# Kernel tuning notes

Hardware: AMD Instinct MI355X
Metric: run time of the kernel (lower is better)

The kernel has to match this reference:

```python
import jax, jax.numpy as jnp
import numpy as np

QN, QP = -8.0, 7.0  # int4: Qn=-2**3, Qp=2**3-1
LOG2E = 1.4426950408889634  # 1/ln(2)

def round_ste(x):
    return x + jax.lax.stop_gradient(jnp.round(x) - x)

def sg(x):
    return jax.lax.stop_gradient(x)

def mean_var_int(x_int, scale=1024):
    """Serial integer running-mean/var recurrence over the last dim.
    x_int: (B,H,N,D) int32. Returns mu (int values, float32) and varn float32, shape (B,H,N,1).
    Matches the torch loop: m_i = m_{i-1} + (x_i-m_{i-1})*int(1024/(i+1))//1024,
    v_i = v_{i-1} + (x_i-m_{i-1})*(x_i-m_i), with m_0=x_0, v_0=0 (same as the general
    recurrence with m_{-1}=v_{-1}=0 since int(1024/1)=1024)."""
    D = x_int.shape[3]
    coef = jnp.array([scale // (i + 1) for i in range(D)], dtype=jnp.int32)
    xt = jnp.moveaxis(x_int, 3, 0)  # (D,B,H,N)
    z = jnp.zeros(x_int.shape[:3], jnp.int32)
    def step(carry, inp):
        m, v = carry
        xi, c = inp
        d = xi - m
        new_m = m + (d * c) // scale  # floor division, matches torch //
        new_v = v + d * (xi - new_m)
        return (new_m, new_v), None
    (m, v), _ = jax.lax.scan(step, (z, z), (xt, coef))
    mu = m[..., None].astype(jnp.float32)
    varn = v[..., None].astype(jnp.float32) / D
    return mu, varn

def q_attention_forward(x0, qkv_w, qkv_b, qkv_alpha, qkv_act_alpha,
                        proj_w, proj_b, proj_alpha, proj_act_alpha,
                        norm_q_w, norm_q_b, norm_k_w, norm_k_b,
                        q_alpha, k_alpha, v_alpha, attn_alpha,
                        num_heads=12):
    B, N, C = x0.shape
    H = num_heads
    hd = C // H
    head_scale = hd ** -0.5

    # input activation quantization (ActQ_v2 then .int())
    a_in = qkv_act_alpha.mean()
    x0_2b = sg(jnp.round(jnp.clip(x0 / a_in, QN, QP)))  # int-valued (B,N,C)

    # int4 qkv weight quantization (per-output-channel alpha), integer GEMM
    w_qkv = sg(jnp.round(jnp.clip(qkv_w / qkv_alpha[:, None], QN, QP)))  # (3C,C)
    qkv = jnp.einsum('bnc,oc->bno', x0_2b, w_qkv)
    bias_i = sg(jnp.trunc(qkv_b / a_in / qkv_alpha))  # bias.int()
    qkv = qkv + bias_i

    qkv = jnp.transpose(qkv.reshape(B, N, 3, H, hd), (2, 0, 3, 1, 4))
    q0, k0, v0 = qkv[0], qkv[1], qkv[2]  # (B,H,N,hd)
    alpha_r = qkv_alpha.reshape(3, H, 1, hd)

    # q branch: scaled integer mean/var norm + scaled quantization
    xq = q0 * alpha_r[0]
    mu_q, var_q = mean_var_int(xq.astype(jnp.int32))
    q1 = (xq - mu_q) / (jnp.sqrt(var_q) + 1e-5)
    aq = q_alpha.mean()
    q2 = sg(jnp.round(jnp.clip((q1 + norm_q_b / norm_q_w) * norm_q_w / aq, QN, QP)))

    # k branch
    xk = k0 * alpha_r[1]
    mu_k, var_k = mean_var_int(xk.astype(jnp.int32))
    k1 = (xk - mu_k) / (jnp.sqrt(var_k) + 1e-5)
    ak = k_alpha.mean()
    k2 = sg(jnp.round(jnp.clip((k1 + norm_k_b / norm_k_w) * norm_k_w / ak, QN, QP)))

    # v branch
    av = v_alpha.mean()
    v2 = sg(jnp.round(jnp.clip(v0 * (a_in * alpha_r[2]) / av, QN, QP)))

    # integer q @ k^T
    qk = jnp.einsum('bhqd,bhkd->bhqk', q2, k2)  # (B,H,N,N)

    # power-of-two softmax approximation: 2^floor(e) * (1 + frac(e))
    s = head_scale * aq * ak
    e = LOG2E * s * qk
    f = jnp.floor(e)
    attn_exp = jnp.exp2(f) * (1.0 + (e - f))
    am = attn_alpha.mean()
    attn_norm = attn_exp / attn_exp.sum(-1, keepdims=True)
    attn2 = sg(jnp.round(jnp.clip(attn_norm / am, QN, QP)))

    x1p = jnp.einsum('bhqk,bhkd->bhqd', attn2, v2)
    x1p = jnp.transpose(x1p, (0, 2, 1, 3)).reshape(B, N, C)

    # proj-act quantization (round_pass STE, no .int() here in torch)
    ap = proj_act_alpha.mean()
    x1_2b = round_ste(jnp.clip(x1p * (am * av) / ap, QN, QP))

    w_p = sg(jnp.round(jnp.clip(proj_w / proj_alpha[:, None], QN, QP)))  # w_q.int()
    x2 = jnp.einsum('bnc,oc->bno', x1_2b, w_p) * proj_alpha * ap + proj_b
    return x2

def setup_inputs() -> dict:
    key = jax.random.key(0)
    ks = jax.random.split(key, 17)
    B, N, C, H = 4, 1024, 768, 12
    u = lambda k, shape, lo, hi: jax.random.uniform(k, shape, jnp.float32, lo, hi)
    return {
        "x0": jax.random.normal(ks[0], (B, N, C), jnp.float32),
        "qkv_w": jax.random.normal(ks[1], (3 * C, C), jnp.float32) * 0.02,
        "qkv_b": jax.random.normal(ks[2], (3 * C,), jnp.float32),
        "qkv_alpha": u(ks[3], (3 * C,), 0.008, 0.012),
        "qkv_act_alpha": u(ks[4], (C,), 0.25, 0.35),
        "proj_w": jax.random.normal(ks[5], (C, C), jnp.float32) * 0.02,
        "proj_b": jax.random.normal(ks[6], (C,), jnp.float32) * 0.02,
        "proj_alpha": u(ks[7], (C,), 0.008, 0.012),
        "proj_act_alpha": u(ks[8], (C,), 0.008, 0.012),
        "norm_q_w": u(ks[9], (C // H,), 0.8, 1.2),
        "norm_q_b": jax.random.normal(ks[10], (C // H,), jnp.float32) * 0.1,
        "norm_k_w": u(ks[11], (C // H,), 0.8, 1.2),
        "norm_k_b": jax.random.normal(ks[12], (C // H,), jnp.float32) * 0.1,
        "q_alpha": u(ks[13], (H,), 0.25, 0.35),
        "k_alpha": u(ks[14], (H,), 0.25, 0.35),
        "v_alpha": u(ks[15], (H,), 0.15, 0.25),
        "attn_alpha": u(ks[16], (H,), 0.0008, 0.0015),
    }

def reference(x0, qkv_w, qkv_b, qkv_alpha, qkv_act_alpha,
              proj_w, proj_b, proj_alpha, proj_act_alpha,
              norm_q_w, norm_q_b, norm_k_w, norm_k_b,
              q_alpha, k_alpha, v_alpha, attn_alpha):
    return q_attention_forward(x0, qkv_w, qkv_b, qkv_alpha, qkv_act_alpha,
                               proj_w, proj_b, proj_alpha, proj_act_alpha,
                               norm_q_w, norm_q_b, norm_k_w, norm_k_b,
                               q_alpha, k_alpha, v_alpha, attn_alpha)
```

## Files before the change

### kernel.cpp

```cpp
#include <hip/hip_runtime.h>

typedef unsigned short u16;
typedef unsigned int u32;
typedef __attribute__((ext_vector_type(8))) u16 u16x8;
typedef __attribute__((ext_vector_type(8))) __bf16 bf16x8;
typedef __attribute__((ext_vector_type(4))) float f32x4;

#define LOG2E_F 1.4426950408889634f

__device__ __forceinline__ u16 f2bf(float f) {
  return (u16)(__float_as_uint(f) >> 16);
}
__device__ __forceinline__ float clip87(float x) {
  return fminf(fmaxf(x, -8.0f), 7.0f);
}

typedef const __attribute__((address_space(1))) u32* gp32;
typedef __attribute__((address_space(3))) u32* lp32;
__device__ __forceinline__ void gl16(const void* g, void* l) {
  __builtin_amdgcn_global_load_lds((gp32)g, (lp32)l, 16, 0, 0);
}

__global__ void k_scalars(const float* __restrict__ qkv_act_alpha,
                          const float* __restrict__ proj_act_alpha,
                          const float* __restrict__ q_alpha,
                          const float* __restrict__ k_alpha,
                          const float* __restrict__ v_alpha,
                          const float* __restrict__ attn_alpha,
                          float* __restrict__ scal) {
  int tid = threadIdx.x;
  int wave = tid >> 6, lane = tid & 63;
  if (wave < 6) {
    const float* src = nullptr; int n = 0;
    switch (wave) {
      case 0: src = qkv_act_alpha;  n = 768; break;
      case 1: src = q_alpha;        n = 12;  break;
      case 2: src = k_alpha;        n = 12;  break;
      case 3: src = v_alpha;        n = 12;  break;
      case 4: src = attn_alpha;     n = 12;  break;
      case 5: src = proj_act_alpha; n = 768; break;
    }
    double s = 0.0;
    for (int i = lane; i < n; i += 64) s += (double)src[i];
    s += __shfl_xor(s, 1);
    s += __shfl_xor(s, 2);
    s += __shfl_xor(s, 4);
    s += __shfl_xor(s, 8);
    s += __shfl_xor(s, 16);
    s += __shfl_xor(s, 32);
    if (lane == 0) scal[wave] = (float)(s / (double)n);
  }
  __syncthreads();
  if (tid == 0) {
    float aq = scal[1], ak = scal[2];
    float s_ = (0.125f * aq) * ak;
    scal[6] = LOG2E_F * s_;
    scal[7] = scal[4] * scal[3];
  }
}

__global__ __launch_bounds__(256) void k_quant_weights(
    const float* __restrict__ qkv_w, const float* __restrict__ qkv_alpha,
    const float* __restrict__ qkv_b, const float* __restrict__ proj_w,
    const float* __restrict__ proj_alpha, const float* __restrict__ scal,
    u16* __restrict__ wq, u16* __restrict__ wp, float* __restrict__ biasi) {
  int idx = blockIdx.x * 256 + threadIdx.x;
  const int T1 = 2304 * 768, T2 = 768 * 768;
  if (idx < T1) {
    int o = idx / 768;
    wq[idx] = f2bf(rintf(clip87(qkv_w[idx] / qkv_alpha[o])));
  } else if (idx < T1 + T2) {
    int j = idx - T1;
    int o = j / 768;
    wp[j] = f2bf(rintf(clip87(proj_w[j] / proj_alpha[o])));
  } else if (idx < T1 + T2 + 2304) {
    int o = idx - T1 - T2;
    biasi[o] = truncf((qkv_b[o] / scal[0]) / qkv_alpha[o]);
  }
}

__global__ __launch_bounds__(256) void k_quant_x0(const float* __restrict__ x0,
                                                  const float* __restrict__ scal,
                                                  u16* __restrict__ x0q) {
  int base = (blockIdx.x * 256 + threadIdx.x) * 8;
  float a = scal[0];
  f32x4 v0 = *(const f32x4*)&x0[base];
  f32x4 v1 = *(const f32x4*)&x0[base + 4];
  u16x8 o;
  #pragma unroll
  for (int j = 0; j < 4; j++) o[j] = f2bf(rintf(clip87(v0[j] / a)));
  #pragma unroll
  for (int j = 0; j < 4; j++) o[4 + j] = f2bf(rintf(clip87(v1[j] / a)));
  *(u16x8*)&x0q[base] = o;
}

#define BUF_A64(c) (smem_u16 + (c) * 4096)
#define BUF_B64(c) (smem_u16 + 8192 + (c) * 4096)

__device__ __forceinline__ void stage64(const u16* gAl, const u16* gBl, int K,
                                        u16* bufA, u16* bufB, int w) {
  gl16(gAl, bufA + (w * 16) * 64);
  gl16(gAl + (size_t)8 * K, bufA + (w * 16 + 8) * 64);
  gl16(gBl, bufB + (w * 16) * 64);
  gl16(gBl + (size_t)8 * K, bufB + (w * 16 + 8) * 64);
}

__device__ __forceinline__ void gemm64(const u16* __restrict__ A,
                                       const u16* __restrict__ Bt, int K,
                                       int m0, int n0, u16* smem_u16,
                                       int lane, int wave, f32x4 acc[2][2]) {
  int rsub = lane >> 3;
  int jsrc = (lane & 7) ^ rsub;
  const u16* gAl = A + (size_t)(m0 + wave * 16 + rsub) * K + jsrc * 8;
  const u16* gBl = Bt + (size_t)(n0 + wave * 16 + rsub) * K + jsrc * 8;

  int arow = (wave >> 1) * 32 + (lane & 15);
  int brow = (wave & 1) * 32 + (lane & 15);
  int nsteps = K / 64;

  stage64(gAl, gBl, K, BUF_A64(0), BUF_B64(0), wave);
  __syncthreads();
  for (int t = 0; t < nsteps; t++) {
    int cur = t & 1;
    if (t + 1 < nsteps)
      stage64(gAl + (t + 1) * 64, gBl + (t + 1) * 64, K,
              BUF_A64(cur ^ 1), BUF_B64(cur ^ 1), wave);
    const u16* bA = BUF_A64(cur);
    const u16* bB = BUF_B64(cur);
    #pragma unroll
    for (int kk = 0; kk < 2; kk++) {
      int jj = ((kk * 4 + (lane >> 4)) ^ (lane & 7)) * 8;
      bf16x8 af0 = *(const bf16x8*)&bA[arow * 64 + jj];
      bf16x8 af1 = *(const bf16x8*)&bA[(arow + 16) * 64 + jj];
      bf16x8 bf0 = *(const bf16x8*)&bB[brow * 64 + jj];
      bf16x8 bf1 = *(const bf16x8*)&bB[(brow + 16) * 64 + jj];
      acc[0][0] = __builtin_amdgcn_mfma_f32_16x16x32_bf16(af0, bf0, acc[0][0], 0, 0, 0);
      acc[0][1] = __builtin_amdgcn_mfma_f32_16x16x32_bf16(af0, bf1, acc[0][1], 0, 0, 0);
      acc[1][0] = __builtin_amdgcn_mfma_f32_16x16x32_bf16(af1, bf0, acc[1][0], 0, 0, 0);
      acc[1][1] = __builtin_amdgcn_mfma_f32_16x16x32_bf16(af1, bf1, acc[1][1], 0, 0, 0);
    }
    __syncthreads();
  }
}

__global__ __launch_bounds__(256) void k_gemm_qkv(
    const u16* __restrict__ A, const u16* __restrict__ Bt,
    const float* __restrict__ biasi, const float* __restrict__ qkv_alpha,
    const float* __restrict__ nqw, const float* __restrict__ nqb,
    const float* __restrict__ nkw, const float* __restrict__ nkb,
    const float* __restrict__ scal,
    u16* __restrict__ q2, u16* __restrict__ k2, u16* __restrict__ v2t) {
  const int K = 768;
  __shared__ __align__(16) char smem[32768];
  u16* smem_u16 = (u16*)smem;
  float* xt = (float*)smem;
  int tid = threadIdx.x;
  int lane = tid & 63, wave = tid >> 6;
  int wr = wave >> 1, wc = wave & 1;
  int m0 = blockIdx.y * 64, n0 = blockIdx.x * 64;

  f32x4 acc[2][2];
  #pragma unroll
  for (int mi = 0; mi < 2; mi++)
    #pragma unroll
    for (int ni = 0; ni < 2; ni++) acc[mi][ni] = (f32x4){0.f, 0.f, 0.f, 0.f};

  gemm64(A, Bt, K, m0, n0, smem_u16, lane, wave, acc);

  int lrow = (lane >> 4) * 4, lcol = lane & 15;
  #pragma unroll
  for (int mi = 0; mi < 2; mi++)
    #pragma unroll
    for (int ni = 0; ni < 2; ni++) {
      int c = wc * 32 + ni * 16 + lcol;
      float bs = biasi[n0 + c];
      #pragma unroll
      for (int rr = 0; rr < 4; rr++) {
        int r = wr * 32 + mi * 16 + lrow + rr;
        xt[r * 65 + c] = acc[mi][ni][rr] + bs;
      }
    }
  __syncthreads();

  int branch = blockIdx.x / 12, h = blockIdx.x % 12;
  int b = m0 >> 10, nb = m0 & 1023;
  if (branch == 2) {
    int d = tid & 63, qr = tid >> 6;
    float av = scal[3];
    float coefv = scal[0] * qkv_alpha[1536 + h * 64 + d];
    u16* dst = v2t + ((size_t)(b * 12 + h) * 64 + d) * 1024 + nb + qr * 16;
    #pragma unroll
    for (int g = 0; g < 2; g++) {
      u16x8 t8;
      #pragma unroll
      for (int j = 0; j < 8; j++) {
        float val = xt[(qr * 16 + g * 8 + j) * 65 + d];
        t8[j] = f2bf(rintf(clip87((val * coefv) / av)));
      }
      *(u16x8*)(dst + g * 8) = t8;
    }
  } else if (tid < 64) {
    int r = tid;
    const float* alph = qkv_alpha + branch * 768 + h * 64;
    const float* wv = branch == 0 ? nqw : nkw;
    const float* bv = branch == 0 ? nqb : nkb;
    float as = branch == 0 ? scal[1] : scal[2];
    float xq[64];
    #pragma unroll
    for (int d = 0; d < 64; d++) xq[d] = xt[r * 65 + d] * alph[d];
    int m = 0, v = 0;
    #pragma unroll
    for (int i = 0; i < 64; i++) {
      int xi = (int)xq[i];
      int dd = xi - m;
      m += (dd * (1024 / (i + 1))) >> 10;
      v += dd * (xi - m);
    }
    float muf = (float)m;
    float den = sqrtf((float)v * 0.015625f) + 1e-5f;
    u16* outp = (branch == 0 ? q2 : k2) + ((size_t)(b * 12 + h) * 1024 + nb + r) * 64;
    #pragma unroll
    for (int g = 0; g < 8; g++) {
      u16x8 t8;
      #pragma unroll
      for (int j = 0; j < 8; j++) {
        int d = g * 8 + j;
        float q1 = (xq[d] - muf) / den;
        float bw = bv[d] / wv[d];
        float t = (q1 + bw) * wv[d] / as;
        t8[j] = f2bf(rintf(clip87(t)));
      }
      *(u16x8*)(outp + g * 8) = t8;
    }
  }
}

__global__ __launch_bounds__(256) void k_gemm_proj(
    const u16* __restrict__ A, const u16* __restrict__ Bt,
    float* __restrict__ Cout, const float* __restrict__ palpha,
    const float* __restrict__ pbias, const float* __restrict__ scal) {
  const int K = 768, N = 768;
  __shared__ __align__(16) char smem[32768];
  u16* smem_u16 = (u16*)smem;
  int tid = threadIdx.x;
  int lane = tid & 63, wave = tid >> 6;
  int wr = wave >> 1, wc = wave & 1;
  int m0 = blockIdx.y * 64, n0 = blockIdx.x * 64;

  f32x4 acc[2][2];
  #pragma unroll
  for (int mi = 0; mi < 2; mi++)
    #pragma unroll
    for (int ni = 0; ni < 2; ni++) acc[mi][ni] = (f32x4){0.f, 0.f, 0.f, 0.f};

  gemm64(A, Bt, K, m0, n0, smem_u16, lane, wave, acc);

  int lrow = (lane >> 4) * 4, lcol = lane & 15;
  float ap = scal[5];
  #pragma unroll
  for (int mi = 0; mi < 2; mi++)
    #pragma unroll
    for (int ni = 0; ni < 2; ni++) {
      int col = n0 + wc * 32 + ni * 16 + lcol;
      float pa = palpha[col], pb = pbias[col];
      #pragma unroll
      for (int rr = 0; rr < 4; rr++) {
        int row = m0 + wr * 32 + mi * 16 + lrow + rr;
        Cout[(size_t)row * N + col] = (acc[mi][ni][rr] * pa) * ap + pb;
      }
    }
}

__global__ __launch_bounds__(256) void k_attn(
    const u16* __restrict__ q2, const u16* __restrict__ k2,
    const u16* __restrict__ v2t, const float* __restrict__ scal,
    u16* __restrict__ x1q) {
  __shared__ __align__(16) u16 lK[2][64 * 72];
  __shared__ __align__(16) u16 lV[2][64 * 72];
  __shared__ __align__(16) u16 lP[64 * 72];
  __shared__ float rs_lds[64];
  int tid = threadIdx.x, lane = tid & 63, wave = tid >> 6;
  int flat = blockIdx.y * gridDim.x + blockIdx.x;
  int wg = (flat & 7) * 96 + (flat >> 3);
  int qt = wg & 15, bh = wg >> 4;
  const float escale = scal[6], am = scal[4], am_av = scal[7], apc = scal[5];

  size_t qrow = (size_t)bh * 1024 + qt * 64 + wave * 16 + (lane & 15);
  bf16x8 qf0 = *(const bf16x8*)(q2 + qrow * 64 + (lane >> 4) * 8);
  bf16x8 qf1 = *(const bf16x8*)(q2 + qrow * 64 + 32 + (lane >> 4) * 8);

  const u16* k2b = k2 + (size_t)bh * 1024 * 64;
  const u16* v2b = v2t + (size_t)bh * 64 * 1024;
  int sr = tid >> 2, sc = (tid & 3) * 16;
  int lofs = sr * 72 + sc;

  double rsum[4] = {0.0, 0.0, 0.0, 0.0};
  {
    const u16* s0 = k2b + (size_t)sr * 64 + sc;
    u16x8 ka = *(const u16x8*)s0, kb = *(const u16x8*)(s0 + 8);
    *(u16x8*)&lK[0][lofs] = ka;
    *(u16x8*)&lK[0][lofs + 8] = kb;
    __syncthreads();
  }
  int cur = 0;
  for (int kt = 0; kt < 16; kt++) {
    u16x8 ka, kb;
    if (kt < 15) {
      const u16* s1 = k2b + (size_t)((kt + 1) * 64 + sr) * 64 + sc;
      ka = *(const u16x8*)s1; kb = *(const u16x8*)(s1 + 8);
    }
    const u16* lKc = lK[cur];
    float part[4] = {0.f, 0.f, 0.f, 0.f};
    #pragma unroll
    for (int ct = 0; ct < 4; ct++) {
      bf16x8 kf0 = *(const bf16x8*)&lKc[(ct * 16 + (lane & 15)) * 72 + (lane >> 4) * 8];
      bf16x8 kf1 = *(const bf16x8*)&lKc[(ct * 16 + (lane & 15)) * 72 + 32 + (lane >> 4) * 8];
      f32x4 s = {0.f, 0.f, 0.f, 0.f};
      s = __builtin_amdgcn_mfma_f32_16x16x32_bf16(qf0, kf0, s, 0, 0, 0);
      s = __builtin_amdgcn_mfma_f32_16x16x32_bf16(qf1, kf1, s, 0, 0, 0);
      #pragma unroll
      for (int rr = 0; rr < 4; rr++) {
        float e = escale * s[rr];
        float f = floorf(e);
        float pe = ldexpf(1.0f + (e - f), (int)f);
        part[rr] += pe;
      }
    }
    #pragma unroll
    for (int rr = 0; rr < 4; rr++) rsum[rr] += (double)part[rr];
    if (kt < 15) {
      *(u16x8*)&lK[cur ^ 1][lofs] = ka;
      *(u16x8*)&lK[cur ^ 1][lofs + 8] = kb;
    }
    __syncthreads();
    cur ^= 1;
  }
  #pragma unroll
  for (int rr = 0; rr < 4; rr++) {
    double s = rsum[rr];
    s += __shfl_xor(s, 1);
    s += __shfl_xor(s, 2);
    s += __shfl_xor(s, 4);
    s += __shfl_xor(s, 8);
    if ((lane & 15) == 0) rs_lds[wave * 16 + (lane >> 4) * 4 + rr] = (float)s;
  }
  __syncthreads();
  float fac[4];
  #pragma unroll
  for (int rr = 0; rr < 4; rr++)
    fac[rr] = 1.0f / (rs_lds[wave * 16 + (lane >> 4) * 4 + rr] * am);

  f32x4 accv[4];
  #pragma unroll
  for (int ct = 0; ct < 4; ct++) accv[ct] = (f32x4){0.f, 0.f, 0.f, 0.f};

  {
    const u16* sk = k2b + (size_t)sr * 64 + sc;
    const u16* sv = v2b + (size_t)sr * 1024 + sc;
    u16x8 ka = *(const u16x8*)sk, kb = *(const u16x8*)(sk + 8);
    u16x8 va = *(const u16x8*)sv, vb = *(const u16x8*)(sv + 8);
    *(u16x8*)&lK[0][lofs] = ka;  *(u16x8*)&lK[0][lofs + 8] = kb;
    *(u16x8*)&lV[0][lofs] = va;  *(u16x8*)&lV[0][lofs + 8] = vb;
    __syncthreads();
  }
  cur = 0;
  for (int kt = 0; kt < 16; kt++) {
    u16x8 ka, kb, va, vb;
    if (kt < 15) {
      const u16* sk = k2b + (size_t)((kt + 1) * 64 + sr) * 64 + sc;
      const u16* sv = v2b + (size_t)sr * 1024 + (kt + 1) * 64 + sc;
      ka = *(const u16x8*)sk; kb = *(const u16x8*)(sk + 8);
      va = *(const u16x8*)sv; vb = *(const u16x8*)(sv + 8);
    }
    const u16* lKc = lK[cur];
    #pragma unroll
    for (int ct = 0; ct < 4; ct++) {
      bf16x8 kf0 = *(const bf16x8*)&lKc[(ct * 16 + (lane & 15)) * 72 + (lane >> 4) * 8];
      bf16x8 kf1 = *(const bf16x8*)&lKc[(ct * 16 + (lane & 15)) * 72 + 32 + (lane >> 4) * 8];
      f32x4 s = {0.f, 0.f, 0.f, 0.f};
      s = __builtin_amdgcn_mfma_f32_16x16x32_bf16(qf0, kf0, s, 0, 0, 0);
      s = __builtin_amdgcn_mfma_f32_16x16x32_bf16(qf1, kf1, s, 0, 0, 0);
      #pragma unroll
      for (int rr = 0; rr < 4; rr++) {
        float e = escale * s[rr];
        float f = floorf(e);
        float pe = ldexpf(1.0f + (e - f), (int)f);
        float a2 = rintf(fminf(pe * fac[rr], 7.0f));
        lP[(wave * 16 + (lane >> 4) * 4 + rr) * 72 + ct * 16 + (lane & 15)] = f2bf(a2);
      }
    }
    if (kt < 15) {
      *(u16x8*)&lK[cur ^ 1][lofs] = ka;  *(u16x8*)&lK[cur ^ 1][lofs + 8] = kb;
      *(u16x8*)&lV[cur ^ 1][lofs] = va;  *(u16x8*)&lV[cur ^ 1][lofs + 8] = vb;
    }
    __syncthreads();
    const u16* lVc = lV[cur];
    bf16x8 pf0 = *(const bf16x8*)&lP[(wave * 16 + (lane & 15)) * 72 + (lane >> 4) * 8];
    bf16x8 pf1 = *(const bf16x8*)&lP[(wave * 16 + (lane & 15)) * 72 + 32 + (lane >> 4) * 8];
    #pragma unroll
    for (int ct = 0; ct < 4; ct++) {
      bf16x8 vf0 = *(const bf16x8*)&lVc[(ct * 16 + (lane & 15)) * 72 + (lane >> 4) * 8];
      bf16x8 vf1 = *(const bf16x8*)&lVc[(ct * 16 + (lane & 15)) * 72 + 32 + (lane >> 4) * 8];
      accv[ct] = __builtin_amdgcn_mfma_f32_16x16x32_bf16(pf0, vf0, accv[ct], 0, 0, 0);
      accv[ct] = __builtin_amdgcn_mfma_f32_16x16x32_bf16(pf1, vf1, accv[ct], 0, 0, 0);
    }
    __syncthreads();
    cur ^= 1;
  }

  int b = bh / 12, h = bh % 12;
  #pragma unroll
  for (int ct = 0; ct < 4; ct++)
    #pragma unroll
    for (int rr = 0; rr < 4; rr++) {
      int qr = qt * 64 + wave * 16 + (lane >> 4) * 4 + rr;
      int col = h * 64 + ct * 16 + (lane & 15);
      float t = (accv[ct][rr] * am_av) / apc;
      x1q[((size_t)b * 1024 + qr) * 768 + col] = f2bf(rintf(clip87(t)));
    }
}

extern "C" void kernel_launch(void* const* d_in, const int* in_sizes, int n_in,
                              void* d_out, int out_size, void* d_ws, size_t ws_size,
                              hipStream_t stream) {
  const float* x0             = (const float*)d_in[0];
  const float* qkv_w          = (const float*)d_in[1];
  const float* qkv_b          = (const float*)d_in[2];
  const float* qkv_alpha      = (const float*)d_in[3];
  const float* qkv_act_alpha  = (const float*)d_in[4];
  const float* proj_w         = (const float*)d_in[5];
  const float* proj_b         = (const float*)d_in[6];
  const float* proj_alpha     = (const float*)d_in[7];
  const float* proj_act_alpha = (const float*)d_in[8];
  const float* nqw            = (const float*)d_in[9];
  const float* nqb            = (const float*)d_in[10];
  const float* nkw            = (const float*)d_in[11];
  const float* nkb            = (const float*)d_in[12];
  const float* q_alpha        = (const float*)d_in[13];
  const float* k_alpha        = (const float*)d_in[14];
  const float* v_alpha        = (const float*)d_in[15];
  const float* attn_alpha     = (const float*)d_in[16];
  float* out = (float*)d_out;

  char* ws = (char*)d_ws;
  size_t off = 0;
  auto alloc = [&](size_t bytes) -> void* {
    off = (off + 255) & ~(size_t)255;
    void* p = ws + off;
    off += bytes;
    return p;
  };
  float* scal = (float*)alloc(64);
  u16* wq     = (u16*)alloc((size_t)2304 * 768 * 2);
  u16* wp     = (u16*)alloc((size_t)768 * 768 * 2);
  float* biasi= (float*)alloc((size_t)2304 * 4);
  u16* x0q    = (u16*)alloc((size_t)4096 * 768 * 2);
  u16* q2     = (u16*)alloc((size_t)48 * 1024 * 64 * 2);
  u16* k2     = (u16*)alloc((size_t)48 * 1024 * 64 * 2);
  u16* v2t    = (u16*)alloc((size_t)48 * 1024 * 64 * 2);
  u16* x1q    = (u16*)alloc((size_t)4096 * 768 * 2);

  k_scalars<<<1, 384, 0, stream>>>(qkv_act_alpha, proj_act_alpha, q_alpha, k_alpha,
                                   v_alpha, attn_alpha, scal);

  int totW = 2304 * 768 + 768 * 768 + 2304;
  k_quant_weights<<<(totW + 255) / 256, 256, 0, stream>>>(qkv_w, qkv_alpha, qkv_b,
                                                          proj_w, proj_alpha, scal,
                                                          wq, wp, biasi);

  k_quant_x0<<<(4096 * 768) / (256 * 8), 256, 0, stream>>>(x0, scal, x0q);

  k_gemm_qkv<<<dim3(36, 64), 256, 0, stream>>>(x0q, wq, biasi, qkv_alpha,
                                               nqw, nqb, nkw, nkb, scal,
                                               q2, k2, v2t);

  k_attn<<<dim3(16, 48), 256, 0, stream>>>(q2, k2, v2t, scal, x1q);

  k_gemm_proj<<<dim3(12, 64), 256, 0, stream>>>(x1q, wp, out, proj_alpha, proj_b, scal);
}
```

Baseline: 209.4 us.

## Transpose score MFMA so lanes own query rows; use per-wave P buffer

Swaps the MFMA operand order so the score tile is computed as K·Qᵀ. Each lane then holds four keys for a single query. Row sums become two cross-lane shuffles instead of a shuffle reduction through shared memory plus a barrier. The softmax tile P goes into a per-wave shared buffer with packed 32-bit writes, which removes one __syncthreads per key tile in the P·V loop. The exp/quantize math is unchanged, with the trade-off of slightly different register and shared-memory access patterns.

Result: faster. 204.2 us (-2.5%).

```diff
diff --git a/kernel.cpp b/kernel.cpp
--- a/kernel.cpp
+++ b/kernel.cpp
@@ -13,6 +13,10 @@
 }
 __device__ __forceinline__ float clip87(float x) {
   return fminf(fmaxf(x, -8.0f), 7.0f);
+}
+__device__ __forceinline__ float pow2exp(float e) {
+  float f = floorf(e);
+  return ldexpf(1.0f + (e - f), (int)f);
 }
 
 typedef const __attribute__((address_space(1))) u32* gp32;
@@ -277,24 +281,25 @@
     u16* __restrict__ x1q) {
   __shared__ __align__(16) u16 lK[2][64 * 72];
   __shared__ __align__(16) u16 lV[2][64 * 72];
-  __shared__ __align__(16) u16 lP[64 * 72];
-  __shared__ float rs_lds[64];
+  __shared__ __align__(16) u16 lP[4][16 * 72];
   int tid = threadIdx.x, lane = tid & 63, wave = tid >> 6;
   int flat = blockIdx.y * gridDim.x + blockIdx.x;
   int wg = (flat & 7) * 96 + (flat >> 3);
   int qt = wg & 15, bh = wg >> 4;
   const float escale = scal[6], am = scal[4], am_av = scal[7], apc = scal[5];
-
-  size_t qrow = (size_t)bh * 1024 + qt * 64 + wave * 16 + (lane & 15);
-  bf16x8 qf0 = *(const bf16x8*)(q2 + qrow * 64 + (lane >> 4) * 8);
-  bf16x8 qf1 = *(const bf16x8*)(q2 + qrow * 64 + 32 + (lane >> 4) * 8);
+  int q = lane & 15, cc = lane >> 4;
+
+  size_t qrow = (size_t)bh * 1024 + qt * 64 + wave * 16 + q;
+  bf16x8 qf0 = *(const bf16x8*)(q2 + qrow * 64 + cc * 8);
+  bf16x8 qf1 = *(const bf16x8*)(q2 + qrow * 64 + 32 + cc * 8);
 
   const u16* k2b = k2 + (size_t)bh * 1024 * 64;
   const u16* v2b = v2t + (size_t)bh * 64 * 1024;
   int sr = tid >> 2, sc = (tid & 3) * 16;
   int lofs = sr * 72 + sc;
-
-  double rsum[4] = {0.0, 0.0, 0.0, 0.0};
+  u16* lPw = lP[wave];
+
+  double rsum = 0.0;
   {
     const u16* s0 = k2b + (size_t)sr * 64 + sc;
     u16x8 ka = *(const u16x8*)s0, kb = *(const u16x8*)(s0 + 8);
@@ -310,24 +315,22 @@
       ka = *(const u16x8*)s1; kb = *(const u16x8*)(s1 + 8);
     }
     const u16* lKc = lK[cur];
-    float part[4] = {0.f, 0.f, 0.f, 0.f};
+    f32x4 st[4];
     #pragma unroll
     for (int ct = 0; ct < 4; ct++) {
-      bf16x8 kf0 = *(const bf16x8*)&lKc[(ct * 16 + (lane & 15)) * 72 + (lane >> 4) * 8];
-      bf16x8 kf1 = *(const bf16x8*)&lKc[(ct * 16 + (lane & 15)) * 72 + 32 + (lane >> 4) * 8];
-      f32x4 s = {0.f, 0.f, 0.f, 0.f};
-      s = __builtin_amdgcn_mfma_f32_16x16x32_bf16(qf0, kf0, s, 0, 0, 0);
-      s = __builtin_amdgcn_mfma_f32_16x16x32_bf16(qf1, kf1, s, 0, 0, 0);
-      #pragma unroll
-      for (int rr = 0; rr < 4; rr++) {
-        float e = escale * s[rr];
-        float f = floorf(e);
-        float pe = ldexpf(1.0f + (e - f), (int)f);
-        part[rr] += pe;
-      }
-    }
-    #pragma unroll
-    for (int rr = 0; rr < 4; rr++) rsum[rr] += (double)part[rr];
+      st[ct] = (f32x4){0.f, 0.f, 0.f, 0.f};
+      bf16x8 kf0 = *(const bf16x8*)&lKc[(ct * 16 + q) * 72 + cc * 8];
+      bf16x8 kf1 = *(const bf16x8*)&lKc[(ct * 16 + q) * 72 + 32 + cc * 8];
+      st[ct] = __builtin_amdgcn_mfma_f32_16x16x32_bf16(kf0, qf0, st[ct], 0, 0, 0);
+      st[ct] = __builtin_amdgcn_mfma_f32_16x16x32_bf16(kf1, qf1, st[ct], 0, 0, 0);
+    }
+    float part = 0.f;
+    #pragma unroll
+    for (int ct = 0; ct < 4; ct++)
+      #pragma unroll
+      for (int rr = 0; rr < 4; rr++)
+        part += pow2exp(escale * st[ct][rr]);
+    rsum += (double)part;
     if (kt < 15) {
       *(u16x8*)&lK[cur ^ 1][lofs] = ka;
       *(u16x8*)&lK[cur ^ 1][lofs + 8] = kb;
@@ -335,20 +338,9 @@
     __syncthreads();
     cur ^= 1;
   }
-  #pragma unroll
-  for (int rr = 0; rr < 4; rr++) {
-    double s = rsum[rr];
-    s += __shfl_xor(s, 1);
-    s += __shfl_xor(s, 2);
-    s += __shfl_xor(s, 4);
-    s += __shfl_xor(s, 8);
-    if ((lane & 15) == 0) rs_lds[wave * 16 + (lane >> 4) * 4 + rr] = (float)s;
-  }
-  __syncthreads();
-  float fac[4];
-  #pragma unroll
-  for (int rr = 0; rr < 4; rr++)
-    fac[rr] = 1.0f / (rs_lds[wave * 16 + (lane >> 4) * 4 + rr] * am);
+  rsum += __shfl_xor(rsum, 16);
+  rsum += __shfl_xor(rsum, 32);
+  float fac = 1.0f / ((float)rsum * am);
 
   f32x4 accv[4];
   #pragma unroll
@@ -373,38 +365,40 @@
       va = *(const u16x8*)sv; vb = *(const u16x8*)(sv + 8);
     }
     const u16* lKc = lK[cur];
+    const u16* lVc = lV[cur];
+    f32x4 st[4];
     #pragma unroll
     for (int ct = 0; ct < 4; ct++) {
-      bf16x8 kf0 = *(const bf16x8*)&lKc[(ct * 16 + (lane & 15)) * 72 + (lane >> 4) * 8];
-      bf16x8 kf1 = *(const bf16x8*)&lKc[(ct * 16 + (lane & 15)) * 72 + 32 + (lane >> 4) * 8];
-      f32x4 s = {0.f, 0.f, 0.f, 0.f};
-      s = __builtin_amdgcn_mfma_f32_16x16x32_bf16(qf0, kf0, s, 0, 0, 0);
-      s = __builtin_amdgcn_mfma_f32_16x16x32_bf16(qf1, kf1, s, 0, 0, 0);
-      #pragma unroll
-      for (int rr = 0; rr < 4; rr++) {
-        float e = escale * s[rr];
-        float f = floorf(e);
-        float pe = ldexpf(1.0f + (e - f), (int)f);
-        float a2 = rintf(fminf(pe * fac[rr], 7.0f));
-        lP[(wave * 16 + (lane >> 4) * 4 + rr) * 72 + ct * 16 + (lane & 15)] = f2bf(a2);
+      st[ct] = (f32x4){0.f, 0.f, 0.f, 0.f};
+      bf16x8 kf0 = *(const bf16x8*)&lKc[(ct * 16 + q) * 72 + cc * 8];
+      bf16x8 kf1 = *(const bf16x8*)&lKc[(ct * 16 + q) * 72 + 32 + cc * 8];
+      st[ct] = __builtin_amdgcn_mfma_f32_16x16x32_bf16(kf0, qf0, st[ct], 0, 0, 0);
+      st[ct] = __builtin_amdgcn_mfma_f32_16x16x32_bf16(kf1, qf1, st[ct], 0, 0, 0);
+    }
+    #pragma unroll
+    for (int ct = 0; ct < 4; ct++) {
+      #pragma unroll
+      for (int i = 0; i < 2; i++) {
+        float a0 = rintf(fminf(pow2exp(escale * st[ct][2 * i]) * fac, 7.0f));
+        float a1 = rintf(fminf(pow2exp(escale * st[ct][2 * i + 1]) * fac, 7.0f));
+        u32 w = (u32)f2bf(a0) | ((u32)f2bf(a1) << 16);
+        *(u32*)&lPw[q * 72 + 16 * ct + 4 * cc + 2 * i] = w;
       }
+    }
+    bf16x8 pf0 = *(const bf16x8*)&lPw[q * 72 + 8 * cc];
+    bf16x8 pf1 = *(const bf16x8*)&lPw[q * 72 + 32 + 8 * cc];
+    #pragma unroll
+    for (int ct = 0; ct < 4; ct++) {
+      bf16x8 vf0 = *(const bf16x8*)&lVc[(ct * 16 + q) * 72 + cc * 8];
+      bf16x8 vf1 = *(const bf16x8*)&lVc[(ct * 16 + q) * 72 + 32 + cc * 8];
+      accv[ct] = __builtin_amdgcn_mfma_f32_16x16x32_bf16(pf0, vf0, accv[ct], 0, 0, 0);
+      accv[ct] = __builtin_amdgcn_mfma_f32_16x16x32_bf16(pf1, vf1, accv[ct], 0, 0, 0);
     }
     if (kt < 15) {
       *(u16x8*)&lK[cur ^ 1][lofs] = ka;  *(u16x8*)&lK[cur ^ 1][lofs + 8] = kb;
       *(u16x8*)&lV[cur ^ 1][lofs] = va;  *(u16x8*)&lV[cur ^ 1][lofs + 8] = vb;
     }
     __syncthreads();
-    const u16* lVc = lV[cur];
-    bf16x8 pf0 = *(const bf16x8*)&lP[(wave * 16 + (lane & 15)) * 72 + (lane >> 4) * 8];
-    bf16x8 pf1 = *(const bf16x8*)&lP[(wave * 16 + (lane & 15)) * 72 + 32 + (lane >> 4) * 8];
-    #pragma unroll
-    for (int ct = 0; ct < 4; ct++) {
-      bf16x8 vf0 = *(const bf16x8*)&lVc[(ct * 16 + (lane & 15)) * 72 + (lane >> 4) * 8];
-      bf16x8 vf1 = *(const bf16x8*)&lVc[(ct * 16 + (lane & 15)) * 72 + 32 + (lane >> 4) * 8];
-      accv[ct] = __builtin_amdgcn_mfma_f32_16x16x32_bf16(pf0, vf0, accv[ct], 0, 0, 0);
-      accv[ct] = __builtin_amdgcn_mfma_f32_16x16x32_bf16(pf1, vf1, accv[ct], 0, 0, 0);
-    }
-    __syncthreads();
     cur ^= 1;
   }
 
@@ -413,8 +407,8 @@
   for (int ct = 0; ct < 4; ct++)
     #pragma unroll
     for (int rr = 0; rr < 4; rr++) {
-      int qr = qt * 64 + wave * 16 + (lane >> 4) * 4 + rr;
-      int col = h * 64 + ct * 16 + (lane & 15);
+      int qr = qt * 64 + wave * 16 + cc * 4 + rr;
+      int col = h * 64 + ct * 16 + q;
       float t = (accv[ct][rr] * am_av) / apc;
       x1q[((size_t)b * 1024 + qr) * 768 + col] = f2bf(rintf(clip87(t)));
     }
```
